# Kernel tuning notes

Measured on AMD Instinct MI355X. Metric: run time of the kernel, lower is better.

The kernel has to match this reference:

```python
import jax, jax.numpy as jnp
import numpy as np

N = 500000   # nodes per batched graph
D = 64       # per-graph node feature dim (encoded_dims // 2)
P = 1000000  # number of interface candidate pairs
ED = 2 * D   # encoded_dims = 128


def setup_inputs() -> dict:
    key = jax.random.key(0)
    k1, k2, k3, k4, k5, k6 = jax.random.split(key, 6)
    graph1_x = jax.random.normal(k1, (N, D), dtype=jnp.float32)
    graph2_x = jax.random.normal(k2, (N, D), dtype=jnp.float32)
    idx_left = jax.random.randint(k3, (P,), 0, N, dtype=jnp.int32).astype(jnp.int64)
    idx_right = jax.random.randint(k4, (P,), 0, N, dtype=jnp.int32).astype(jnp.int64)
    W1 = jax.random.normal(k5, (ED, ED), dtype=jnp.float32) * (1.0 / np.sqrt(ED))
    b1 = jnp.zeros((ED,), dtype=jnp.float32)
    W2 = jax.random.normal(k6, (1, ED), dtype=jnp.float32) * (1.0 / np.sqrt(ED))
    b2 = jnp.zeros((1,), dtype=jnp.float32)
    return {"graph1_x": graph1_x, "graph2_x": graph2_x,
            "idx_left": idx_left, "idx_right": idx_right,
            "W1": W1, "b1": b1, "W2": W2, "b2": b2}


def reference(graph1_x, graph2_x, idx_left, idx_right, W1, b1, W2, b2):
    # Gather interface node features from both encoded graphs.
    left = graph1_x[idx_left]    # [P, D]
    right = graph2_x[idx_right]  # [P, D]
    x = jnp.concatenate([left, right], axis=1)  # [P, 2D]
    # top_net: Linear -> ReLU -> Dropout(eval: identity) -> Linear
    h = jax.nn.relu(x @ W1.T + b1)  # [P, ED]
    out = h @ W2.T + b2             # [P, 1]
    return out
```

## Files before the change

kernel.cpp:

```cpp
#include <hip/hip_runtime.h>
#include <hip/hip_bf16.h>


typedef __bf16 bf16x8 __attribute__((ext_vector_type(8)));
typedef float f32x16 __attribute__((ext_vector_type(16)));

__device__ __forceinline__ unsigned f2bf(float f) {
  union { float f; unsigned u; } v;
  v.f = f;
  unsigned u = v.u;
  return (u + 0x7fffu + ((u >> 16) & 1u)) >> 16;
}

__global__ __launch_bounds__(256) void w1_frag_kernel(
    const float* __restrict__ W1, uint4* __restrict__ w1f) {
  int t = blockIdx.x * 256 + threadIdx.x;
  int lane = t & 63;
  int nt = (t >> 6) & 3;
  int ks = t >> 8;
  int n = lane & 31, h = lane >> 5;
  const float4* src =
      (const float4*)(W1 + ((nt * 32 + n) * 128 + ks * 16 + h * 8));
  float4 a = src[0], b = src[1];
  uint4 o;
  o.x = f2bf(a.x) | (f2bf(a.y) << 16);
  o.y = f2bf(a.z) | (f2bf(a.w) << 16);
  o.z = f2bf(b.x) | (f2bf(b.y) << 16);
  o.w = f2bf(b.z) | (f2bf(b.w) << 16);
  w1f[t] = o;
}

#define LDS_STRIDE 136

__global__ __launch_bounds__(256, 3) void pip_main_kernel(
    const float* __restrict__ g1, const float* __restrict__ g2,
    const int* __restrict__ il, const int* __restrict__ ir,
    const bf16x8* __restrict__ w1f,
    const float* __restrict__ b1, const float* __restrict__ w2,
    const float* __restrict__ b2,
    float* __restrict__ out, int P) {
  __shared__ unsigned short A[128 * LDS_STRIDE];

  const int t = threadIdx.x;
  const int lane = t & 63;
  const int w = t >> 6;
  const int pair0 = blockIdx.x * 128;

  const int sub = lane & 15;
  const int g = lane >> 4;
  const int side = g & 1;
  const int pairB = w * 2 + (g >> 1);
  const float* feat = side ? g2 : g1;
  const int* idxarr = side ? ir : il;

  int idxv[16];
#pragma unroll
  for (int j = 0; j < 16; ++j) {
    int gp = pair0 + j * 8 + pairB;
    int pidx = (gp < P) ? gp : (P - 1);
    idxv[j] = idxarr[pidx];
  }
  asm volatile("" : "+v"(idxv[0]), "+v"(idxv[1]), "+v"(idxv[2]), "+v"(idxv[3]),
                    "+v"(idxv[4]), "+v"(idxv[5]), "+v"(idxv[6]), "+v"(idxv[7]),
                    "+v"(idxv[8]), "+v"(idxv[9]), "+v"(idxv[10]), "+v"(idxv[11]),
                    "+v"(idxv[12]), "+v"(idxv[13]), "+v"(idxv[14]), "+v"(idxv[15]));

#pragma unroll
  for (int b = 0; b < 2; ++b) {
    float4 v[8];
#pragma unroll
    for (int u = 0; u < 8; ++u)
      v[u] = *(const float4*)(feat + (size_t)idxv[b * 8 + u] * 64 + sub * 4);
    asm volatile("" :
        "+v"(v[0].x), "+v"(v[0].y), "+v"(v[0].z), "+v"(v[0].w),
        "+v"(v[1].x), "+v"(v[1].y), "+v"(v[1].z), "+v"(v[1].w),
        "+v"(v[2].x), "+v"(v[2].y), "+v"(v[2].z), "+v"(v[2].w),
        "+v"(v[3].x), "+v"(v[3].y), "+v"(v[3].z), "+v"(v[3].w),
        "+v"(v[4].x), "+v"(v[4].y), "+v"(v[4].z), "+v"(v[4].w),
        "+v"(v[5].x), "+v"(v[5].y), "+v"(v[5].z), "+v"(v[5].w),
        "+v"(v[6].x), "+v"(v[6].y), "+v"(v[6].z), "+v"(v[6].w),
        "+v"(v[7].x), "+v"(v[7].y), "+v"(v[7].z), "+v"(v[7].w));
#pragma unroll
    for (int u = 0; u < 8; ++u) {
      int j = b * 8 + u;
      unsigned lo = f2bf(v[u].x) | (f2bf(v[u].y) << 16);
      unsigned hi = f2bf(v[u].z) | (f2bf(v[u].w) << 16);
      *(uint2*)(A + (j * 8 + pairB) * LDS_STRIDE + side * 64 + sub * 4) =
          make_uint2(lo, hi);
    }
  }
  __syncthreads();

  const int n = lane & 31;
  const int h = lane >> 5;

  f32x16 acc[4];
#pragma unroll
  for (int nt = 0; nt < 4; ++nt)
#pragma unroll
    for (int i = 0; i < 16; ++i) acc[nt][i] = 0.0f;

  const unsigned short* Arow = A + (w * 32 + n) * LDS_STRIDE + h * 8;
#pragma unroll
  for (int ks = 0; ks < 8; ++ks) {
    bf16x8 af = *(const bf16x8*)(Arow + ks * 16);
#pragma unroll
    for (int nt = 0; nt < 4; ++nt) {
      bf16x8 bfr = w1f[(ks * 4 + nt) * 64 + lane];
      acc[nt] = __builtin_amdgcn_mfma_f32_32x32x16_bf16(af, bfr, acc[nt], 0, 0, 0);
    }
  }

  float b1v[4], w2v[4];
#pragma unroll
  for (int nt = 0; nt < 4; ++nt) {
    b1v[nt] = b1[nt * 32 + n];
    w2v[nt] = w2[nt * 32 + n];
  }
  const float bias2 = b2[0];

#pragma unroll
  for (int r = 0; r < 16; ++r) {
    float s = 0.0f;
#pragma unroll
    for (int nt = 0; nt < 4; ++nt) {
      float vv = acc[nt][r] + b1v[nt];
      vv = fmaxf(vv, 0.0f);
      s = fmaf(vv, w2v[nt], s);
    }
    s += __shfl_xor(s, 1);
    s += __shfl_xor(s, 2);
    s += __shfl_xor(s, 4);
    s += __shfl_xor(s, 8);
    s += __shfl_xor(s, 16);
    if (n == 0) {
      int row = (r & 3) + 8 * (r >> 2) + 4 * h;
      int gp = pair0 + w * 32 + row;
      if (gp < P) out[gp] = s + bias2;
    }
  }
}

extern "C" void kernel_launch(void* const* d_in, const int* in_sizes, int n_in,
                              void* d_out, int out_size, void* d_ws, size_t ws_size,
                              hipStream_t stream) {
  const float* g1 = (const float*)d_in[0];
  const float* g2 = (const float*)d_in[1];
  const int* il = (const int*)d_in[2];
  const int* ir = (const int*)d_in[3];
  const float* W1 = (const float*)d_in[4];
  const float* b1 = (const float*)d_in[5];
  const float* w2 = (const float*)d_in[6];
  const float* b2 = (const float*)d_in[7];
  float* out = (float*)d_out;
  const int P = out_size;

  w1_frag_kernel<<<8, 256, 0, stream>>>(W1, (uint4*)d_ws);

  const int nblocks = (P + 127) / 128;
  pip_main_kernel<<<nblocks, 256, 0, stream>>>(
      g1, g2, il, ir, (const bf16x8*)d_ws, b1, w2, b2, out, P);
}
```

Measured before the change: 339.3 us.

## Pre-convert node feature tables to bf16 before gathering pairs

Adds a streaming pass that converts both node feature tables to bf16 in workspace, then gathers half-size rows in a new main kernel with higher occupancy. The random gather traffic is halved and the per-element conversion leaves the main kernel. The cost is an extra full read and write of both tables on every call, and the path only runs if the workspace is large enough; otherwise it falls back to the fp32 kernel.

Measured after the change: 382.9 us. 1.13x slower.

```diff
diff --git a/kernel.cpp b/kernel.cpp
--- a/kernel.cpp
+++ b/kernel.cpp
@@ -30,9 +30,126 @@
   w1f[t] = o;
 }
 
+__global__ __launch_bounds__(256) void cvt_bf16_kernel(
+    const float4* __restrict__ a, const float4* __restrict__ b,
+    uint2* __restrict__ da, uint2* __restrict__ db, int n4) {
+  const int stride = gridDim.x * 256;
+  for (int i = blockIdx.x * 256 + threadIdx.x; i < 2 * n4; i += stride) {
+    const float4* s;
+    uint2* d;
+    int k;
+    if (i < n4) { s = a; d = da; k = i; }
+    else        { s = b; d = db; k = i - n4; }
+    float4 v = s[k];
+    d[k] = make_uint2(f2bf(v.x) | (f2bf(v.y) << 16),
+                      f2bf(v.z) | (f2bf(v.w) << 16));
+  }
+}
+
 #define LDS_STRIDE 136
 
-__global__ __launch_bounds__(256, 3) void pip_main_kernel(
+__global__ __launch_bounds__(256, 4) void pip_main_bf16(
+    const uint4* __restrict__ gl, const uint4* __restrict__ gr,
+    const int* __restrict__ il, const int* __restrict__ ir,
+    const bf16x8* __restrict__ w1f,
+    const float* __restrict__ b1, const float* __restrict__ w2,
+    const float* __restrict__ b2,
+    float* __restrict__ out, int P) {
+  __shared__ unsigned short A[128 * LDS_STRIDE];
+
+  const int t = threadIdx.x;
+  const int lane = t & 63;
+  const int w = t >> 6;
+  const int pair0 = blockIdx.x * 128;
+
+  const int sub = lane & 7;
+  const int grp = lane >> 3;
+  const int side = grp & 1;
+  const int pOff = grp >> 1;
+  const uint4* feat = side ? gr : gl;
+  const int* idxarr = side ? ir : il;
+
+  int idxv[8];
+#pragma unroll
+  for (int j = 0; j < 8; ++j) {
+    int gp = pair0 + j * 16 + w * 4 + pOff;
+    int pidx = (gp < P) ? gp : (P - 1);
+    idxv[j] = idxarr[pidx];
+  }
+  asm volatile("" : "+v"(idxv[0]), "+v"(idxv[1]), "+v"(idxv[2]), "+v"(idxv[3]),
+                    "+v"(idxv[4]), "+v"(idxv[5]), "+v"(idxv[6]), "+v"(idxv[7]));
+
+  uint4 v[8];
+#pragma unroll
+  for (int j = 0; j < 8; ++j)
+    v[j] = feat[(size_t)idxv[j] * 8 + sub];
+  asm volatile("" :
+      "+v"(v[0].x), "+v"(v[0].y), "+v"(v[0].z), "+v"(v[0].w),
+      "+v"(v[1].x), "+v"(v[1].y), "+v"(v[1].z), "+v"(v[1].w),
+      "+v"(v[2].x), "+v"(v[2].y), "+v"(v[2].z), "+v"(v[2].w),
+      "+v"(v[3].x), "+v"(v[3].y), "+v"(v[3].z), "+v"(v[3].w),
+      "+v"(v[4].x), "+v"(v[4].y), "+v"(v[4].z), "+v"(v[4].w),
+      "+v"(v[5].x), "+v"(v[5].y), "+v"(v[5].z), "+v"(v[5].w),
+      "+v"(v[6].x), "+v"(v[6].y), "+v"(v[6].z), "+v"(v[6].w),
+      "+v"(v[7].x), "+v"(v[7].y), "+v"(v[7].z), "+v"(v[7].w));
+#pragma unroll
+  for (int j = 0; j < 8; ++j) {
+    int pair = j * 16 + w * 4 + pOff;
+    *(uint4*)(A + pair * LDS_STRIDE + side * 64 + sub * 8) = v[j];
+  }
+  __syncthreads();
+
+  const int n = lane & 31;
+  const int h = lane >> 5;
+
+  f32x16 acc[4];
+#pragma unroll
+  for (int nt = 0; nt < 4; ++nt)
+#pragma unroll
+    for (int i = 0; i < 16; ++i) acc[nt][i] = 0.0f;
+
+  const unsigned short* Arow = A + (w * 32 + n) * LDS_STRIDE + h * 8;
+#pragma unroll
+  for (int ks = 0; ks < 8; ++ks) {
+    bf16x8 af = *(const bf16x8*)(Arow + ks * 16);
+#pragma unroll
+    for (int nt = 0; nt < 4; ++nt) {
+      bf16x8 bfr = w1f[(ks * 4 + nt) * 64 + lane];
+      acc[nt] = __builtin_amdgcn_mfma_f32_32x32x16_bf16(af, bfr, acc[nt], 0, 0, 0);
+    }
+  }
+
+  float b1v[4], w2v[4];
+#pragma unroll
+  for (int nt = 0; nt < 4; ++nt) {
+    b1v[nt] = b1[nt * 32 + n];
+    w2v[nt] = w2[nt * 32 + n];
+  }
+  const float bias2 = b2[0];
+
+#pragma unroll
+  for (int r = 0; r < 16; ++r) {
+    float s = 0.0f;
+#pragma unroll
+    for (int nt = 0; nt < 4; ++nt) {
+      float vv = acc[nt][r] + b1v[nt];
+      vv = fmaxf(vv, 0.0f);
+      s = fmaf(vv, w2v[nt], s);
+    }
+    s += __shfl_xor(s, 1);
+    s += __shfl_xor(s, 2);
+    s += __shfl_xor(s, 4);
+    s += __shfl_xor(s, 8);
+    s += __shfl_xor(s, 16);
+    if (n == 0) {
+      int row = (r & 3) + 8 * (r >> 2) + 4 * h;
+      int gp = pair0 + w * 32 + row;
+      if (gp < P) out[gp] = s + bias2;
+    }
+  }
+}
+
+__global__ __launch_bounds__(256, 3) void pip_main_f32(
     const float* __restrict__ g1, const float* __restrict__ g2,
     const int* __restrict__ il, const int* __restrict__ ir,
     const bf16x8* __restrict__ w1f,
@@ -60,34 +177,13 @@
     int pidx = (gp < P) ? gp : (P - 1);
     idxv[j] = idxarr[pidx];
   }
-  asm volatile("" : "+v"(idxv[0]), "+v"(idxv[1]), "+v"(idxv[2]), "+v"(idxv[3]),
-                    "+v"(idxv[4]), "+v"(idxv[5]), "+v"(idxv[6]), "+v"(idxv[7]),
-                    "+v"(idxv[8]), "+v"(idxv[9]), "+v"(idxv[10]), "+v"(idxv[11]),
-                    "+v"(idxv[12]), "+v"(idxv[13]), "+v"(idxv[14]), "+v"(idxv[15]));
-
-#pragma unroll
-  for (int b = 0; b < 2; ++b) {
-    float4 v[8];
-#pragma unroll
-    for (int u = 0; u < 8; ++u)
-      v[u] = *(const float4*)(feat + (size_t)idxv[b * 8 + u] * 64 + sub * 4);
-    asm volatile("" :
-        "+v"(v[0].x), "+v"(v[0].y), "+v"(v[0].z), "+v"(v[0].w),
-        "+v"(v[1].x), "+v"(v[1].y), "+v"(v[1].z), "+v"(v[1].w),
-        "+v"(v[2].x), "+v"(v[2].y), "+v"(v[2].z), "+v"(v[2].w),
-        "+v"(v[3].x), "+v"(v[3].y), "+v"(v[3].z), "+v"(v[3].w),
-        "+v"(v[4].x), "+v"(v[4].y), "+v"(v[4].z), "+v"(v[4].w),
-        "+v"(v[5].x), "+v"(v[5].y), "+v"(v[5].z), "+v"(v[5].w),
-        "+v"(v[6].x), "+v"(v[6].y), "+v"(v[6].z), "+v"(v[6].w),
-        "+v"(v[7].x), "+v"(v[7].y), "+v"(v[7].z), "+v"(v[7].w));
-#pragma unroll
-    for (int u = 0; u < 8; ++u) {
-      int j = b * 8 + u;
-      unsigned lo = f2bf(v[u].x) | (f2bf(v[u].y) << 16);
-      unsigned hi = f2bf(v[u].z) | (f2bf(v[u].w) << 16);
-      *(uint2*)(A + (j * 8 + pairB) * LDS_STRIDE + side * 64 + sub * 4) =
-          make_uint2(lo, hi);
-    }
+#pragma unroll
+  for (int j = 0; j < 16; ++j) {
+    float4 v = *(const float4*)(feat + (size_t)idxv[j] * 64 + sub * 4);
+    unsigned lo = f2bf(v.x) | (f2bf(v.y) << 16);
+    unsigned hi = f2bf(v.z) | (f2bf(v.w) << 16);
+    *(uint2*)(A + (j * 8 + pairB) * LDS_STRIDE + side * 64 + sub * 4) =
+        make_uint2(lo, hi);
   }
   __syncthreads();
 
@@ -157,7 +253,22 @@
 
   w1_frag_kernel<<<8, 256, 0, stream>>>(W1, (uint4*)d_ws);
 
+  const size_t sz1 = (size_t)in_sizes[0] * 2;
+  const size_t need = 32768 + sz1 + (size_t)in_sizes[1] * 2;
   const int nblocks = (P + 127) / 128;
-  pip_main_kernel<<<nblocks, 256, 0, stream>>>(
-      g1, g2, il, ir, (const bf16x8*)d_ws, b1, w2, b2, out, P);
-}
+
+  if (ws_size >= need) {
+    char* wsc = (char*)d_ws;
+    uint2* gl = (uint2*)(wsc + 32768);
+    uint2* gr = (uint2*)(wsc + 32768 + sz1);
+    const int n4 = in_sizes[0] / 4;
+    cvt_bf16_kernel<<<8192, 256, 0, stream>>>(
+        (const float4*)g1, (const float4*)g2, gl, gr, n4);
+    pip_main_bf16<<<nblocks, 256, 0, stream>>>(
+        (const uint4*)gl, (const uint4*)gr, il, ir, (const bf16x8*)d_ws,
+        b1, w2, b2, out, P);
+  } else {
+    pip_main_f32<<<nblocks, 256, 0, stream>>>(
+        g1, g2, il, ir, (const bf16x8*)d_ws, b1, w2, b2, out, P);
+  }
+}
```
